# Performance work log

Measured on AMD Instinct MI355X. Metric: run time of the kernel, lower is better.

## Reference

```python
import jax, jax.numpy as jnp
import numpy as np


def _conv(x, w, b=None, pad=0):
    # x: [N,C,H,W], w: [O,I,kh,kw]
    out = jax.lax.conv_general_dilated(
        x, w, window_strides=(1, 1), padding=[(pad, pad), (pad, pad)],
        dimension_numbers=('NCHW', 'OIHW', 'NCHW'))
    if b is not None:
        out = out + b[None, :, None, None]
    return out


def _sift128(patch):
    """Differentiable SIFT descriptor on [M,1,24,24] -> [M,128].
    Sobel gradients -> 8-bin hard-argmax orientation histogram weighted by
    gradient magnitude -> 4x4 grid of 6x6 cell sums -> L2 normalize -> **0.9."""
    sx = jnp.array([[-1., 0., 1.], [-2., 0., 2.], [-1., 0., 1.]], dtype=patch.dtype)
    gw = jnp.stack([sx, sx.T])[:, None]                     # [2,1,3,3] (Ix, Iy filters)
    g = _conv(patch, gw, pad=1)                             # [M,2,24,24]
    Ix, Iy = g[:, 0], g[:, 1]
    mag = jnp.sqrt(Ix * Ix + Iy * Iy + 1e-12)               # [M,24,24]
    ang = jnp.pi / 8 + jnp.arange(8, dtype=patch.dtype) * (jnp.pi / 4)
    # projection of gradient onto each of 8 orientation unit vectors
    cosines = (jnp.cos(ang)[None, :, None, None] * Ix[:, None]
               + jnp.sin(ang)[None, :, None, None] * Iy[:, None])  # [M,8,24,24]
    mask = (cosines == cosines.max(axis=1, keepdims=True)).astype(patch.dtype)
    hist = mask * mag[:, None]                              # [M,8,24,24] soft-binned magnitudes
    M = hist.shape[0]
    cells = hist.reshape(M, 8, 4, 6, 4, 6).sum(axis=(3, 5))  # [M,8,4,4] cell accumulation
    feat = cells.reshape(M, 128)
    feat = feat / (jnp.linalg.norm(feat, axis=1, keepdims=True) + 1e-8)
    return (feat + 1e-8) ** 0.9


def setup_inputs() -> dict:
    key = jax.random.key(0)
    ks = jax.random.split(key, 4)
    x = jax.random.normal(ks[0], (8192, 784), dtype=jnp.float32)
    W1 = jax.random.normal(ks[1], (32, 1, 3, 3), dtype=jnp.float32) * 0.1
    b1 = jnp.zeros((32,), jnp.float32)
    W2 = jax.random.normal(ks[2], (3, 32, 3, 3), dtype=jnp.float32) * 0.05
    b2 = jnp.zeros((3,), jnp.float32)
    Wl = jax.random.normal(ks[3], (10, 384), dtype=jnp.float32) * 0.05
    bl = jnp.zeros((10,), jnp.float32)
    return {"x": x, "W1": W1, "b1": b1, "W2": W2, "b2": b2, "Wl": Wl, "bl": bl}


def reference(x, W1, b1, W2, b2, Wl, bl):
    x = x.reshape(-1, 1, 28, 28)
    x = jax.nn.relu(_conv(x, W1, b1))          # [N,32,26,26]
    x = _conv(x, W2, b2)                       # [N,3,24,24]
    N = x.shape[0]
    # per-channel SIFT loop == batched SIFT over N*3 single-channel patches
    feats = _sift128(x.reshape(N * 3, 1, 24, 24)).reshape(N, 3 * 128)
    logits = feats @ Wl.T + bl                 # [N,10]
    return jax.nn.softmax(jax.nn.relu(logits), axis=1)
```

## Files before the change

### kernel.cpp

```cpp
#include <hip/hip_runtime.h>
#include <math.h>

#define TPB 576

__device__ __forceinline__ float f4c(const float4 v, int p) {
    return (p == 0) ? v.x : ((p == 1) ? v.y : v.z);
}

__global__ __launch_bounds__(TPB) void fused_pipeline(
    const float* __restrict__ x,
    const float* __restrict__ W1,
    const float* __restrict__ b1,
    const float* __restrict__ W2,
    const float* __restrict__ b2,
    const float* __restrict__ Wl,
    const float* __restrict__ bl,
    float* __restrict__ out)
{
    __shared__ float  xs[784];
    __shared__ float4 buf[2][676];
    __shared__ float4 s2v[26 * 26];
    __shared__ float  hist[384];
    __shared__ float  nrm[3];
    __shared__ float  lg[10];

    const int n = blockIdx.x;
    const int t = threadIdx.x;

    for (int i = t; i < 784; i += TPB) xs[i] = x[n * 784 + i];
    for (int i = t; i < 676; i += TPB) s2v[i] = make_float4(0.f, 0.f, 0.f, 0.f);
    if (t < 384) hist[t] = 0.f;
    __syncthreads();

    const int p0i = t / 26, p0j = t % 26;
    float xn[9];
#pragma unroll
    for (int q = 0; q < 9; ++q)
        xn[q] = xs[(p0i + q / 3) * 28 + (p0j + q % 3)];
    const int p1  = 576 + t;
    const int p1i = p1 / 26, p1j = p1 % 26;

    const int i2 = t / 24, j2 = t % 24;

    float acc[3] = {0.f, 0.f, 0.f};

#pragma unroll 1
    for (int cg = 0; cg < 8; ++cg) {
        const int c0 = cg * 4;
        {
            float4 v;
            float* vp = (float*)&v;
#pragma unroll
            for (int cc = 0; cc < 4; ++cc) {
                const float* w = W1 + (c0 + cc) * 9;
                float s = b1[c0 + cc];
#pragma unroll
                for (int q = 0; q < 9; ++q) s += w[q] * xn[q];
                vp[cc] = fmaxf(s, 0.f);
            }
            buf[cg & 1][t] = v;
        }
        if (t < 100) {
            float4 v;
            float* vp = (float*)&v;
#pragma unroll
            for (int cc = 0; cc < 4; ++cc) {
                const float* w = W1 + (c0 + cc) * 9;
                float s = b1[c0 + cc];
#pragma unroll
                for (int q = 0; q < 9; ++q)
                    s += w[q] * xs[(p1i + q / 3) * 28 + (p1j + q % 3)];
                vp[cc] = fmaxf(s, 0.f);
            }
            buf[cg & 1][p1] = v;
        }
        __syncthreads();
        const float4* bp = buf[cg & 1];
#pragma unroll
        for (int di = 0; di < 3; ++di) {
            const float4 a0 = bp[(i2 + di) * 26 + j2 + 0];
            const float4 a1 = bp[(i2 + di) * 26 + j2 + 1];
            const float4 a2 = bp[(i2 + di) * 26 + j2 + 2];
#pragma unroll
            for (int k = 0; k < 3; ++k) {
                const float* w = W2 + k * 288 + c0 * 9 + di * 3;
                acc[k] += w[0] * a0.x + w[9]  * a0.y + w[18] * a0.z + w[27] * a0.w
                        + w[1] * a1.x + w[10] * a1.y + w[19] * a1.z + w[28] * a1.w
                        + w[2] * a2.x + w[11] * a2.y + w[20] * a2.z + w[29] * a2.w;
            }
        }
    }

    s2v[(i2 + 1) * 26 + (j2 + 1)] =
        make_float4(acc[0] + b2[0], acc[1] + b2[1], acc[2] + b2[2], 0.f);
    __syncthreads();

    {
        const float C0 = 0.92387953f;
        const float C1 = 0.38268343f;
        const int cell = (i2 / 6) * 4 + (j2 / 6);

        float4 Pr[3][3];
#pragma unroll
        for (int r = 0; r < 3; ++r)
#pragma unroll
            for (int c = 0; c < 3; ++c)
                Pr[r][c] = s2v[(i2 + r) * 26 + (j2 + c)];

#pragma unroll
        for (int p = 0; p < 3; ++p) {
            const float p00 = f4c(Pr[0][0], p), p01 = f4c(Pr[0][1], p), p02 = f4c(Pr[0][2], p);
            const float p10 = f4c(Pr[1][0], p),                         p12 = f4c(Pr[1][2], p);
            const float p20 = f4c(Pr[2][0], p), p21 = f4c(Pr[2][1], p), p22 = f4c(Pr[2][2], p);
            const float Ix = (p02 - p00) + 2.f * (p12 - p10) + (p22 - p20);
            const float Iy = (p20 - p00) + 2.f * (p21 - p01) + (p22 - p02);
            const float mag = sqrtf(Ix * Ix + Iy * Iy + 1e-12f);
            float cs[8];
            cs[0] =  C0 * Ix + C1 * Iy;
            cs[1] =  C1 * Ix + C0 * Iy;
            cs[2] = -C1 * Ix + C0 * Iy;
            cs[3] = -C0 * Ix + C1 * Iy;
            cs[4] = -C0 * Ix - C1 * Iy;
            cs[5] = -C1 * Ix - C0 * Iy;
            cs[6] =  C1 * Ix - C0 * Iy;
            cs[7] =  C0 * Ix - C1 * Iy;
            float cmax = cs[0];
#pragma unroll
            for (int k = 1; k < 8; ++k) cmax = fmaxf(cmax, cs[k]);
#pragma unroll
            for (int k = 0; k < 8; ++k)
                if (cs[k] == cmax)
                    atomicAdd(&hist[p * 128 + k * 16 + cell], mag);
        }
    }
    __syncthreads();

    if (t < 192) {
        const int p = t >> 6, l = t & 63;
        const float v0 = hist[p * 128 + l], v1 = hist[p * 128 + l + 64];
        float s = v0 * v0 + v1 * v1;
#pragma unroll
        for (int off = 32; off; off >>= 1) s += __shfl_down(s, off);
        if (l == 0) nrm[p] = sqrtf(s) + 1e-8f;
    }
    __syncthreads();

    if (t < 384) {
        const int p = t >> 7;
        const float v = hist[t] / nrm[p] + 1e-8f;
        hist[t] = powf(v, 0.9f);
    }
    __syncthreads();

    if (t < 160) {
        const int o = t >> 4, l = t & 15;
        const float* w = Wl + o * 384;
        float s = 0.f;
#pragma unroll 4
        for (int q = l; q < 384; q += 16) s += hist[q] * w[q];
#pragma unroll
        for (int off = 8; off; off >>= 1) s += __shfl_down(s, off, 16);
        if (l == 0) lg[o] = s + bl[o];
    }
    __syncthreads();

    if (t == 0) {
        float z[10], m = 0.f, ssum = 0.f;
#pragma unroll
        for (int o = 0; o < 10; ++o) { z[o] = fmaxf(lg[o], 0.f); m = fmaxf(m, z[o]); }
#pragma unroll
        for (int o = 0; o < 10; ++o) { z[o] = expf(z[o] - m); ssum += z[o]; }
        const float inv = 1.f / ssum;
#pragma unroll
        for (int o = 0; o < 10; ++o) lg[o] = z[o] * inv;
    }
    __syncthreads();
    if (t < 10) out[n * 10 + t] = lg[t];
}

extern "C" void kernel_launch(void* const* d_in, const int* in_sizes, int n_in,
                              void* d_out, int out_size, void* d_ws, size_t ws_size,
                              hipStream_t stream) {
    const float* x  = (const float*)d_in[0];
    const float* W1 = (const float*)d_in[1];
    const float* b1 = (const float*)d_in[2];
    const float* W2 = (const float*)d_in[3];
    const float* b2 = (const float*)d_in[4];
    const float* Wl = (const float*)d_in[5];
    const float* bl = (const float*)d_in[6];
    float* out = (float*)d_out;
    const int N = in_sizes[0] / 784;
    fused_pipeline<<<N, TPB, 0, stream>>>(x, W1, b1, W2, b2, Wl, bl, out);
}
```

Before: 478.4 us.

## Replace histogram atomics with mask-and-reduce, overlay shared buffers, vectorize loads

```diff
diff --git a/kernel.cpp b/kernel.cpp
--- a/kernel.cpp
+++ b/kernel.cpp
@@ -17,19 +17,27 @@
     const float* __restrict__ bl,
     float* __restrict__ out)
 {
-    __shared__ float  xs[784];
-    __shared__ float4 buf[2][676];
-    __shared__ float4 s2v[26 * 26];
-    __shared__ float  hist[384];
-    __shared__ float  nrm[3];
-    __shared__ float  lg[10];
+    __shared__ __align__(16) char arena[37200];
+    float4* const s2v  = (float4*)(arena);
+    float*  const xs   = (float*)(arena + 10816);
+    float4* const buf  = (float4*)(arena + 13952);
+    float4* const pm   = (float4*)(arena + 13952);
+    float*  const hist = (float*)(arena + 35584);
+    float*  const nrm  = (float*)(arena + 37120);
+    float*  const lg   = (float*)(arena + 37136);
 
     const int n = blockIdx.x;
     const int t = threadIdx.x;
 
-    for (int i = t; i < 784; i += TPB) xs[i] = x[n * 784 + i];
-    for (int i = t; i < 676; i += TPB) s2v[i] = make_float4(0.f, 0.f, 0.f, 0.f);
-    if (t < 384) hist[t] = 0.f;
+    if (t < 196) ((float4*)xs)[t] = ((const float4*)(x + n * 784))[t];
+    if (t < 100) {
+        int idx;
+        if (t < 26)      idx = t;
+        else if (t < 52) idx = 650 + (t - 26);
+        else if (t < 76) idx = (t - 52 + 1) * 26;
+        else             idx = (t - 76 + 1) * 26 + 25;
+        s2v[idx] = make_float4(0.f, 0.f, 0.f, 0.f);
+    }
     __syncthreads();
 
     const int p0i = t / 26, p0j = t % 26;
@@ -37,58 +45,82 @@
 #pragma unroll
     for (int q = 0; q < 9; ++q)
         xn[q] = xs[(p0i + q / 3) * 28 + (p0j + q % 3)];
-    const int p1  = 576 + t;
+    const int p1 = 576 + t;
     const int p1i = p1 / 26, p1j = p1 % 26;
+    float xn2[9];
+    if (t < 100) {
+#pragma unroll
+        for (int q = 0; q < 9; ++q)
+            xn2[q] = xs[(p1i + q / 3) * 28 + (p1j + q % 3)];
+    }
 
     const int i2 = t / 24, j2 = t % 24;
-
     float acc[3] = {0.f, 0.f, 0.f};
 
-#pragma unroll 1
-    for (int cg = 0; cg < 8; ++cg) {
-        const int c0 = cg * 4;
-        {
-            float4 v;
-            float* vp = (float*)&v;
+    const float4* const rb0 = buf + i2 * 26 + j2;
+    const float4* const rb1 = rb0 + 676;
+    float4* const wb0 = buf + t;
+    float4* const wb1 = wb0 + 676;
+    float4* const wq0 = buf + p1;
+    float4* const wq1 = wq0 + 676;
+
+    auto conv1_step = [&](int c0, float4* wdst, float4* wdst2) {
+        float4 v;
+        float* vp = (float*)&v;
+#pragma unroll
+        for (int cc = 0; cc < 4; ++cc) {
+            const float* w = W1 + (c0 + cc) * 9;
+            float s = b1[c0 + cc];
+#pragma unroll
+            for (int q = 0; q < 9; ++q) s = fmaf(w[q], xn[q], s);
+            vp[cc] = fmaxf(s, 0.f);
+        }
+        *wdst = v;
+        if (t < 100) {
+            float4 v2;
+            float* vp2 = (float*)&v2;
 #pragma unroll
             for (int cc = 0; cc < 4; ++cc) {
                 const float* w = W1 + (c0 + cc) * 9;
                 float s = b1[c0 + cc];
 #pragma unroll
-                for (int q = 0; q < 9; ++q) s += w[q] * xn[q];
-                vp[cc] = fmaxf(s, 0.f);
+                for (int q = 0; q < 9; ++q) s = fmaf(w[q], xn2[q], s);
+                vp2[cc] = fmaxf(s, 0.f);
             }
-            buf[cg & 1][t] = v;
-        }
-        if (t < 100) {
-            float4 v;
-            float* vp = (float*)&v;
-#pragma unroll
-            for (int cc = 0; cc < 4; ++cc) {
-                const float* w = W1 + (c0 + cc) * 9;
-                float s = b1[c0 + cc];
-#pragma unroll
-                for (int q = 0; q < 9; ++q)
-                    s += w[q] * xs[(p1i + q / 3) * 28 + (p1j + q % 3)];
-                vp[cc] = fmaxf(s, 0.f);
-            }
-            buf[cg & 1][p1] = v;
-        }
-        __syncthreads();
-        const float4* bp = buf[cg & 1];
+            *wdst2 = v2;
+        }
+    };
+
+    auto conv2_step = [&](int c0, const float4* r) {
 #pragma unroll
         for (int di = 0; di < 3; ++di) {
-            const float4 a0 = bp[(i2 + di) * 26 + j2 + 0];
-            const float4 a1 = bp[(i2 + di) * 26 + j2 + 1];
-            const float4 a2 = bp[(i2 + di) * 26 + j2 + 2];
+            const float4 a0 = r[di * 26 + 0];
+            const float4 a1 = r[di * 26 + 1];
+            const float4 a2 = r[di * 26 + 2];
 #pragma unroll
             for (int k = 0; k < 3; ++k) {
                 const float* w = W2 + k * 288 + c0 * 9 + di * 3;
-                acc[k] += w[0] * a0.x + w[9]  * a0.y + w[18] * a0.z + w[27] * a0.w
-                        + w[1] * a1.x + w[10] * a1.y + w[19] * a1.z + w[28] * a1.w
-                        + w[2] * a2.x + w[11] * a2.y + w[20] * a2.z + w[29] * a2.w;
+                float s = acc[k];
+                s = fmaf(w[0],  a0.x, s); s = fmaf(w[9],  a0.y, s);
+                s = fmaf(w[18], a0.z, s); s = fmaf(w[27], a0.w, s);
+                s = fmaf(w[1],  a1.x, s); s = fmaf(w[10], a1.y, s);
+                s = fmaf(w[19], a1.z, s); s = fmaf(w[28], a1.w, s);
+                s = fmaf(w[2],  a2.x, s); s = fmaf(w[11], a2.y, s);
+                s = fmaf(w[20], a2.z, s); s = fmaf(w[29], a2.w, s);
+                acc[k] = s;
             }
         }
+    };
+
+#pragma unroll 1
+    for (int cc2 = 0; cc2 < 4; ++cc2) {
+        const int c0 = cc2 * 8;
+        conv1_step(c0, wb0, wq0);
+        __syncthreads();
+        conv2_step(c0, rb0);
+        conv1_step(c0 + 4, wb1, wq1);
+        __syncthreads();
+        conv2_step(c0 + 4, rb1);
     }
 
     s2v[(i2 + 1) * 26 + (j2 + 1)] =
@@ -96,17 +128,17 @@
     __syncthreads();
 
     {
-        const float C0 = 0.92387953f;
-        const float C1 = 0.38268343f;
-        const int cell = (i2 / 6) * 4 + (j2 / 6);
-
+        const float C0c = 0.92387953f;
+        const float C1c = 0.38268343f;
+        const float4* P = s2v + i2 * 26 + j2;
         float4 Pr[3][3];
 #pragma unroll
         for (int r = 0; r < 3; ++r)
 #pragma unroll
-            for (int c = 0; c < 3; ++c)
-                Pr[r][c] = s2v[(i2 + r) * 26 + (j2 + c)];
-
+            for (int c = 0; c < 3; ++c) Pr[r][c] = P[r * 26 + c];
+
+        float mg[3];
+        unsigned int msk = 0u;
 #pragma unroll
         for (int p = 0; p < 3; ++p) {
             const float p00 = f4c(Pr[0][0], p), p01 = f4c(Pr[0][1], p), p02 = f4c(Pr[0][2], p);
@@ -114,31 +146,52 @@
             const float p20 = f4c(Pr[2][0], p), p21 = f4c(Pr[2][1], p), p22 = f4c(Pr[2][2], p);
             const float Ix = (p02 - p00) + 2.f * (p12 - p10) + (p22 - p20);
             const float Iy = (p20 - p00) + 2.f * (p21 - p01) + (p22 - p02);
-            const float mag = sqrtf(Ix * Ix + Iy * Iy + 1e-12f);
+            mg[p] = sqrtf(Ix * Ix + Iy * Iy + 1e-12f);
             float cs[8];
-            cs[0] =  C0 * Ix + C1 * Iy;
-            cs[1] =  C1 * Ix + C0 * Iy;
-            cs[2] = -C1 * Ix + C0 * Iy;
-            cs[3] = -C0 * Ix + C1 * Iy;
-            cs[4] = -C0 * Ix - C1 * Iy;
-            cs[5] = -C1 * Ix - C0 * Iy;
-            cs[6] =  C1 * Ix - C0 * Iy;
-            cs[7] =  C0 * Ix - C1 * Iy;
-            float cmax = cs[0];
-#pragma unroll
-            for (int k = 1; k < 8; ++k) cmax = fmaxf(cmax, cs[k]);
+            cs[0] =  C0c * Ix + C1c * Iy;
+            cs[1] =  C1c * Ix + C0c * Iy;
+            cs[2] = -C1c * Ix + C0c * Iy;
+            cs[3] = -C0c * Ix + C1c * Iy;
+            cs[4] = -C0c * Ix - C1c * Iy;
+            cs[5] = -C1c * Ix - C0c * Iy;
+            cs[6] =  C1c * Ix - C0c * Iy;
+            cs[7] =  C0c * Ix - C1c * Iy;
+            float cm = cs[0];
+#pragma unroll
+            for (int k = 1; k < 8; ++k) cm = fmaxf(cm, cs[k]);
 #pragma unroll
             for (int k = 0; k < 8; ++k)
-                if (cs[k] == cmax)
-                    atomicAdd(&hist[p * 128 + k * 16 + cell], mag);
-        }
+                if (cs[k] == cm) msk |= (1u << (p * 8 + k));
+        }
+        pm[i2 * 25 + j2] = make_float4(mg[0], mg[1], mg[2], __uint_as_float(msk));
+    }
+    __syncthreads();
+
+    if (t < 128) {
+        const int k = t >> 4, cell = t & 15;
+        const int r0 = (cell >> 2) * 6, c0p = (cell & 3) * 6;
+        const float4* cp = pm + r0 * 25 + c0p;
+        float s0 = 0.f, s1 = 0.f, s2 = 0.f;
+#pragma unroll
+        for (int r = 0; r < 6; ++r)
+#pragma unroll
+            for (int c = 0; c < 6; ++c) {
+                const float4 v = cp[r * 25 + c];
+                const unsigned int m = __float_as_uint(v.w);
+                s0 += (m & (1u <<  k))       ? v.x : 0.f;
+                s1 += (m & (1u << (8 + k)))  ? v.y : 0.f;
+                s2 += (m & (1u << (16 + k))) ? v.z : 0.f;
+            }
+        hist[      k * 16 + cell] = s0;
+        hist[128 + k * 16 + cell] = s1;
+        hist[256 + k * 16 + cell] = s2;
     }
     __syncthreads();
 
     if (t < 192) {
         const int p = t >> 6, l = t & 63;
-        const float v0 = hist[p * 128 + l], v1 = hist[p * 128 + l + 64];
-        float s = v0 * v0 + v1 * v1;
+        const float2 v = ((const float2*)(hist + p * 128))[l];
+        float s = v.x * v.x + v.y * v.y;
 #pragma unroll
         for (int off = 32; off; off >>= 1) s += __shfl_down(s, off);
         if (l == 0) nrm[p] = sqrtf(s) + 1e-8f;
@@ -146,18 +199,21 @@
     __syncthreads();
 
     if (t < 384) {
-        const int p = t >> 7;
-        const float v = hist[t] / nrm[p] + 1e-8f;
-        hist[t] = powf(v, 0.9f);
+        const float v = hist[t] / nrm[t >> 7] + 1e-8f;
+        hist[t] = __expf(0.9f * __logf(v));
     }
     __syncthreads();
 
     if (t < 160) {
         const int o = t >> 4, l = t & 15;
-        const float* w = Wl + o * 384;
+        const float4* hv = (const float4*)hist + l * 6;
+        const float4* wv = (const float4*)(Wl + o * 384) + l * 6;
         float s = 0.f;
-#pragma unroll 4
-        for (int q = l; q < 384; q += 16) s += hist[q] * w[q];
+#pragma unroll
+        for (int q = 0; q < 6; ++q) {
+            const float4 h = hv[q], w = wv[q];
+            s += h.x * w.x + h.y * w.y + h.z * w.z + h.w * w.w;
+        }
 #pragma unroll
         for (int off = 8; off; off >>= 1) s += __shfl_down(s, off, 16);
         if (l == 0) lg[o] = s + bl[o];
@@ -169,7 +225,7 @@
 #pragma unroll
         for (int o = 0; o < 10; ++o) { z[o] = fmaxf(lg[o], 0.f); m = fmaxf(m, z[o]); }
 #pragma unroll
-        for (int o = 0; o < 10; ++o) { z[o] = expf(z[o] - m); ssum += z[o]; }
+        for (int o = 0; o < 10; ++o) { z[o] = __expf(z[o] - m); ssum += z[o]; }
         const float inv = 1.f / ssum;
 #pragma unroll
         for (int o = 0; o < 10; ++o) lg[o] = z[o] * inv;
```

Measured after the change: 488.0 us. +2.0%, slower.
